# Performance work log

Hardware: AMD Instinct MI355X
Metric: run time of the kernel (lower is better)

## Reference

```python
import jax, jax.numpy as jnp
import numpy as np

B, S, D = 8, 2048, 768

def setup_inputs() -> dict:
    key = jax.random.key(0)
    k1, k2, k3, k4 = jax.random.split(key, 4)
    x = jax.random.normal(k1, (B, S, D), dtype=jnp.float32)
    # torch Linear stores weight as [out, in] and computes x @ W^T; we store
    # pre-transposed [in, out] matrices so forward is x @ W.
    scale = 1.0 / np.sqrt(D)
    wq = jax.random.normal(k2, (D, D), dtype=jnp.float32) * scale
    wk = jax.random.normal(k3, (D, D), dtype=jnp.float32) * scale
    wv = jax.random.normal(k4, (D, D), dtype=jnp.float32) * scale
    return {"x": x, "wq": wq, "wk": wk, "wv": wv}

def reference(x, wq, wk, wv):
    d_out = wq.shape[1]
    q = jnp.einsum('bsd,de->bse', x, wq)
    k = jnp.einsum('bsd,de->bse', x, wk)
    v = jnp.einsum('bsd,de->bse', x, wv)
    # causal scores: note source scales by sqrt(d_out), not per-head dim
    scores = jnp.einsum('bqe,bke->bqk', q, k) / jnp.sqrt(jnp.float32(d_out))
    S_len = x.shape[1]
    causal = jnp.tril(jnp.ones((S_len, S_len), dtype=bool))  # True = keep
    scores = jnp.where(causal[None, :, :], scores, -jnp.inf)
    attn = jax.nn.softmax(scores, axis=-1)
    # dropout rate = 0.0 -> identity
    out = jnp.einsum('bqk,bke->bqe', attn, v)
    return out
```

## Files before the change

### kernel.cpp

```cpp
#include <hip/hip_runtime.h>
#include <hip/hip_bf16.h>

#define DI 768
#define SS 2048
#define QK_ELEMS ((size_t)16384 * 768)

typedef float f32x4 __attribute__((ext_vector_type(4)));
typedef short s16x8 __attribute__((ext_vector_type(8)));
typedef short s16x4 __attribute__((ext_vector_type(4)));

static __device__ __forceinline__ unsigned short f2bf(float f) {
    union { float f; unsigned int u; } a; a.f = f;
    unsigned int r = (a.u + 0x7FFFu + ((a.u >> 16) & 1u)) >> 16;
    return (unsigned short)r;
}

#define GLOAD_LDS16(SRC, DST) \
    __builtin_amdgcn_global_load_lds((const __attribute__((address_space(1))) unsigned int*)(SRC), \
                                     (__attribute__((address_space(3))) unsigned int*)(DST), 16, 0, 0)

__global__ __launch_bounds__(256) void conv_kernel(
    const float* __restrict__ x, unsigned short* __restrict__ xb)
{
    const size_t i = ((size_t)blockIdx.x * 256 + threadIdx.x) * 8;
    float4 a = *(const float4*)(x + i);
    float4 c = *(const float4*)(x + i + 4);
    ushort4 u0, u1;
    u0.x = f2bf(a.x); u0.y = f2bf(a.y); u0.z = f2bf(a.z); u0.w = f2bf(a.w);
    u1.x = f2bf(c.x); u1.y = f2bf(c.y); u1.z = f2bf(c.z); u1.w = f2bf(c.w);
    *(ushort4*)(xb + i) = u0;
    *(ushort4*)(xb + i + 4) = u1;
}

__global__ __launch_bounds__(256) void convw_kernel(
    const float* __restrict__ wq, const float* __restrict__ wk,
    const float* __restrict__ wv, unsigned short* __restrict__ wtb)
{
    __shared__ float tile[64][65];
    const int which = blockIdx.z;
    const float* w = (which == 0) ? wq : (which == 1) ? wk : wv;
    unsigned short* o = wtb + (size_t)which * DI * DI;
    const int k0 = blockIdx.x * 64, n0 = blockIdx.y * 64;
    const int tid = threadIdx.x;
    #pragma unroll
    for (int i = 0; i < 16; ++i) {
        int idx = tid + i * 256;
        int rr = idx >> 6, cc = idx & 63;
        tile[rr][cc] = w[(size_t)(k0 + rr) * DI + n0 + cc];
    }
    __syncthreads();
    #pragma unroll
    for (int i = 0; i < 16; ++i) {
        int idx = tid + i * 256;
        int rr = idx >> 6, cc = idx & 63;
        o[(size_t)(n0 + rr) * DI + k0 + cc] = f2bf(tile[cc][rr]);
    }
}

__global__ __launch_bounds__(256) void proj_kernel(
    const unsigned short* __restrict__ xb, const unsigned short* __restrict__ wtb,
    unsigned short* __restrict__ ws)
{
    __shared__ unsigned short As[128 * 32];
    __shared__ unsigned short Bs[128 * 32];

    const int which = blockIdx.z;
    const unsigned short* wt = wtb + (size_t)which * DI * DI;
    const int n0 = blockIdx.x * 128;
    const int m0 = blockIdx.y * 128;
    const int tid = threadIdx.x;
    const int lane = tid & 63, wid = tid >> 6;
    const int wr = wid >> 1, wc = wid & 1;
    const int r = lane & 15, g = lane >> 4;

    const int arow_l = lane >> 2;
    const int asrc_l = (((lane & 3) * 16) ^ ((arow_l & 1) << 5)) >> 1;

    f32x4 acc[4][4];
    #pragma unroll
    for (int i = 0; i < 4; ++i)
        #pragma unroll
        for (int j = 0; j < 4; ++j) acc[i][j] = (f32x4){0.f, 0.f, 0.f, 0.f};

    for (int k0 = 0; k0 < DI; k0 += 32) {
        #pragma unroll
        for (int ii = 0; ii < 2; ++ii) {
            const int idx = wid * 2 + ii;
            GLOAD_LDS16(xb + (size_t)(m0 + idx * 16 + arow_l) * DI + k0 + asrc_l,
                        &As[idx * 512]);
            GLOAD_LDS16(wt + (size_t)(n0 + idx * 16 + arow_l) * DI + k0 + asrc_l,
                        &Bs[idx * 512]);
        }
        __syncthreads();
        s16x8 af[4], bfr[4];
        #pragma unroll
        for (int fr = 0; fr < 4; ++fr) {
            const int arow = wr * 64 + fr * 16 + r;
            af[fr] = *(const s16x8*)((const char*)As + arow * 64 + ((g * 16) ^ ((arow & 1) << 5)));
        }
        #pragma unroll
        for (int cf = 0; cf < 4; ++cf) {
            const int brow = wc * 64 + cf * 16 + r;
            bfr[cf] = *(const s16x8*)((const char*)Bs + brow * 64 + ((g * 16) ^ ((brow & 1) << 5)));
        }
        #pragma unroll
        for (int fr = 0; fr < 4; ++fr)
            #pragma unroll
            for (int cf = 0; cf < 4; ++cf)
                acc[fr][cf] = __builtin_amdgcn_mfma_f32_16x16x32_bf16(af[fr], bfr[cf], acc[fr][cf], 0, 0, 0);
        __syncthreads();
    }

    if (which == 0) {
        const float scale = 0.03608439182435161f;
        unsigned short* O = ws;
        #pragma unroll
        for (int fr = 0; fr < 4; ++fr)
            #pragma unroll
            for (int cf = 0; cf < 4; ++cf) {
                int row = m0 + wr * 64 + fr * 16 + g * 4;
                int col = n0 + wc * 64 + cf * 16 + r;
                #pragma unroll
                for (int jj = 0; jj < 4; ++jj) {
                    int q = row + jj;
                    O[((size_t)(q >> 5) * 96 + (col >> 3)) * 256 + (q & 31) * 8 + (col & 7)]
                        = f2bf(acc[fr][cf][jj] * scale);
                }
            }
    } else if (which == 1) {
        unsigned short* O = ws + QK_ELEMS;
        #pragma unroll
        for (int fr = 0; fr < 4; ++fr)
            #pragma unroll
            for (int cf = 0; cf < 4; ++cf) {
                int row = m0 + wr * 64 + fr * 16 + g * 4;
                int col = n0 + wc * 64 + cf * 16 + r;
                #pragma unroll
                for (int jj = 0; jj < 4; ++jj) {
                    int s = row + jj;
                    O[((size_t)(s >> 6) * 96 + (col >> 3)) * 512 + (s & 63) * 8 + (col & 7)]
                        = f2bf(acc[fr][cf][jj]);
                }
            }
    } else {
        unsigned short* O = ws + 2 * QK_ELEMS;
        #pragma unroll
        for (int fr = 0; fr < 4; ++fr)
            #pragma unroll
            for (int cf = 0; cf < 4; ++cf) {
                int row = m0 + wr * 64 + fr * 16 + g * 4;
                int bb = row >> 11;
                int st = (row & 2047) >> 4;
                int et = ((n0 + wc * 64) >> 4) + cf;
                ushort4 pk;
                pk.x = f2bf(acc[fr][cf][0]); pk.y = f2bf(acc[fr][cf][1]);
                pk.z = f2bf(acc[fr][cf][2]); pk.w = f2bf(acc[fr][cf][3]);
                *(ushort4*)&O[(((size_t)bb * 128 + st) * 48 + et) * 256 + lane * 4] = pk;
            }
    }
}

__global__ __launch_bounds__(512, 1) void attn_kernel(
    const unsigned short* __restrict__ ws, float* __restrict__ out)
{
    __shared__ unsigned short Ks[96 * 512];
    __shared__ unsigned short Qs[96 * 256];
    __shared__ unsigned short P_lds[2048];
    __shared__ float redm[128];

    const int id = blockIdx.x;
    const int b = id & 7;
    const int a = id >> 3;
    const int tid = threadIdx.x;
    const int wid = tid >> 6, lane = tid & 63;
    const int qsel = wid >> 2;
    const int wv = wid & 3;
    const int r = lane & 15, g = lane >> 4;
    const int et0 = wid * 6;
    const int rw = wv * 16 + r;

    const unsigned short* Qb = ws + (size_t)b * SS * DI;
    const unsigned short* Kb = ws + QK_ELEMS + (size_t)b * SS * DI;
    const unsigned short* Vf = ws + 2 * QK_ELEMS + (size_t)b * 128 * 48 * 256;
    float* Ob = out + (size_t)b * SS * DI;
    const char* KsB = (const char*)Ks;
    const char* QsB = (const char*)Qs;
    const int kfb = g * 1024 + rw * 16;
    const int qfb = g * 512 + (qsel * 16 + r) * 16;

#define STAGEK(KT) do { \
        const size_t sbase_ = (size_t)(KT) * 64 * DI; \
        _Pragma("unroll") \
        for (int i_ = 0; i_ < 12; ++i_) { \
            const int idx_ = wid * 12 + i_; \
            GLOAD_LDS16(Kb + sbase_ + idx_ * 512 + lane * 8, &Ks[idx_ * 512]); \
        } \
    } while (0)

#define RAWBAR() do { \
        asm volatile("s_waitcnt lgkmcnt(0)" ::: "memory"); \
        __builtin_amdgcn_sched_barrier(0); \
        __builtin_amdgcn_s_barrier(); \
        __builtin_amdgcn_sched_barrier(0); \
    } while (0)

    for (int pp = 0; pp < 2; ++pp) {
        const int jbase = pp ? (126 - 2 * a) : (2 * a);
        const int q0 = (jbase + qsel) * 16;
        const int nt0 = (jbase * 16 + 79) >> 6;
        const int ntmax = ((jbase + 1) * 16 + 79) >> 6;
        const int nt_own = qsel ? ntmax : nt0;

        {
            const size_t qsb = (size_t)jbase * 16 * DI;
            #pragma unroll
            for (int i_ = 0; i_ < 6; ++i_) {
                const int idx_ = wid * 6 + i_;
                GLOAD_LDS16(Qb + qsb + idx_ * 512 + lane * 8, &Qs[idx_ * 512]);
            }
        }
        STAGEK(0);

        f32x4 acc[2][6];
        #pragma unroll
        for (int qs = 0; qs < 2; ++qs)
            #pragma unroll
            for (int cf = 0; cf < 6; ++cf) acc[qs][cf] = (f32x4){0.f, 0.f, 0.f, 0.f};
        float m0 = -1e30f, m1 = -1e30f, lp = 0.f;

        for (int kt = 0; kt < ntmax; ++kt) {
            const int k0 = kt * 64;
            const bool act0 = kt < nt0;
            const bool act_own = kt < nt_own;
            __syncthreads();

            s16x4 va[4][6];
            const size_t vbase = ((size_t)(k0 >> 4) * 48 + et0) * 256 + lane * 4;
            #pragma unroll
            for (int ks = 0; ks < 4; ++ks)
                #pragma unroll
                for (int cf = 0; cf < 6; ++cf)
                    va[ks][cf] = *(const s16x4*)(Vf + vbase + (size_t)ks * 48 * 256 + cf * 256);

            f32x4 s = {0.f, 0.f, 0.f, 0.f};
            if (act_own) {
                f32x4 sa = {0,0,0,0}, sb = {0,0,0,0};
                __builtin_amdgcn_s_setprio(1);
                #pragma unroll
                for (int t = 0; t < 24; t += 2) {
                    s16x8 ka  = *(const s16x8*)(KsB + kfb + t * 4096);
                    s16x8 kb2 = *(const s16x8*)(KsB + kfb + t * 4096 + 4096);
                    s16x8 qa  = *(const s16x8*)(QsB + qfb + t * 2048);
                    s16x8 qb2 = *(const s16x8*)(QsB + qfb + t * 2048 + 2048);
                    sa = __builtin_amdgcn_mfma_f32_16x16x32_bf16(ka,  qa,  sa, 0, 0, 0);
                    sb = __builtin_amdgcn_mfma_f32_16x16x32_bf16(kb2, qb2, sb, 0, 0, 0);
                }
                __builtin_amdgcn_s_setprio(0);
                #pragma unroll
                for (int jj = 0; jj < 4; ++jj) s[jj] = sa[jj] + sb[jj];
                if (k0 + 64 > q0) {
                    #pragma unroll
                    for (int jj = 0; jj < 4; ++jj)
                        if (k0 + 16 * wv + 4 * g + jj > q0 + r) s[jj] = -1e30f;
                }
                float v = fmaxf(fmaxf(s[0], s[1]), fmaxf(s[2], s[3]));
                v = fmaxf(v, __shfl_xor(v, 16));
                v = fmaxf(v, __shfl_xor(v, 32));
                if (lane < 16) redm[qsel * 64 + wv * 16 + lane] = v;
            }
            RAWBAR();

            if (kt + 1 < ntmax) STAGEK(kt + 1);

            {
                float vm1 = fmaxf(fmaxf(redm[64 + r], redm[80 + r]),
                                  fmaxf(redm[96 + r], redm[112 + r]));
                float vm0 = act0 ? fmaxf(fmaxf(redm[r], redm[16 + r]),
                                         fmaxf(redm[32 + r], redm[48 + r])) : -1e30f;
                bool need = __any(vm1 > m1 + 8.0f) || (act0 && __any(vm0 > m0 + 8.0f));
                if (need) {
                    const float mn0 = fmaxf(m0, vm0), mn1 = fmaxf(m1, vm1);
                    const float a0 = __expf(m0 - mn0), a1 = __expf(m1 - mn1);
                    m0 = mn0; m1 = mn1;
                    lp *= qsel ? a1 : a0;
                    float al0[4], al1[4];
                    #pragma unroll
                    for (int jj = 0; jj < 4; ++jj) {
                        al0[jj] = __shfl(a0, 4 * g + jj);
                        al1[jj] = __shfl(a1, 4 * g + jj);
                    }
                    #pragma unroll
                    for (int cf = 0; cf < 6; ++cf)
                        #pragma unroll
                        for (int jj = 0; jj < 4; ++jj) {
                            acc[0][cf][jj] *= al0[jj];
                            acc[1][cf][jj] *= al1[jj];
                        }
                }
                if (act_own) {
                    const float mo = qsel ? m1 : m0;
                    s16x4 pw;
                    #pragma unroll
                    for (int jj = 0; jj < 4; ++jj) {
                        float p = __expf(s[jj] - mo);
                        lp += p;
                        pw[jj] = (short)f2bf(p);
                    }
                    *(s16x4*)&P_lds[qsel * 1024 + wv * 256 + r * 16 + g * 4] = pw;
                }
            }
            RAWBAR();

            {
                s16x4 pa0[4], pa1[4];
                #pragma unroll
                for (int ks = 0; ks < 4; ++ks) {
                    pa0[ks] = *(const s16x4*)&P_lds[ks * 256 + r * 16 + g * 4];
                    pa1[ks] = *(const s16x4*)&P_lds[1024 + ks * 256 + r * 16 + g * 4];
                }
                __builtin_amdgcn_s_setprio(1);
                if (act0) {
                    #pragma unroll
                    for (int cf = 0; cf < 6; ++cf)
                        #pragma unroll
                        for (int ks = 0; ks < 4; ++ks)
                            acc[0][cf] = __builtin_amdgcn_mfma_f32_16x16x16bf16_1k(pa0[ks], va[ks][cf], acc[0][cf], 0, 0, 0);
                }
                #pragma unroll
                for (int cf = 0; cf < 6; ++cf)
                    #pragma unroll
                    for (int ks = 0; ks < 4; ++ks)
                        acc[1][cf] = __builtin_amdgcn_mfma_f32_16x16x16bf16_1k(pa1[ks], va[ks][cf], acc[1][cf], 0, 0, 0);
                __builtin_amdgcn_s_setprio(0);
            }
        }
        lp += __shfl_xor(lp, 16);
        lp += __shfl_xor(lp, 32);
        if (lane < 16) redm[qsel * 64 + wv * 16 + lane] = lp;
        __syncthreads();
        const float lt0 = redm[r] + redm[16 + r] + redm[32 + r] + redm[48 + r];
        const float lt1 = redm[64 + r] + redm[80 + r] + redm[96 + r] + redm[112 + r];
        const float li0 = 1.0f / lt0, li1 = 1.0f / lt1;
        float lv0[4], lv1[4];
        #pragma unroll
        for (int jj = 0; jj < 4; ++jj) {
            lv0[jj] = __shfl(li0, 4 * g + jj);
            lv1[jj] = __shfl(li1, 4 * g + jj);
        }
        #pragma unroll
        for (int cf = 0; cf < 6; ++cf)
            #pragma unroll
            for (int jj = 0; jj < 4; ++jj) {
                Ob[(size_t)(jbase * 16 + 4 * g + jj) * DI + wid * 96 + cf * 16 + r] = acc[0][cf][jj] * lv0[jj];
                Ob[(size_t)((jbase + 1) * 16 + 4 * g + jj) * DI + wid * 96 + cf * 16 + r] = acc[1][cf][jj] * lv1[jj];
            }
        __syncthreads();
    }
#undef STAGEK
#undef RAWBAR
}

extern "C" void kernel_launch(void* const* d_in, const int* in_sizes, int n_in,
                              void* d_out, int out_size, void* d_ws, size_t ws_size,
                              hipStream_t stream) {
    const float* x  = (const float*)d_in[0];
    const float* wq = (const float*)d_in[1];
    const float* wk = (const float*)d_in[2];
    const float* wv = (const float*)d_in[3];
    unsigned short* ws = (unsigned short*)d_ws;
    float* out = (float*)d_out;
    unsigned short* xb  = (unsigned short*)d_out;
    unsigned short* wtb = (unsigned short*)d_out + QK_ELEMS;

    conv_kernel<<<(int)(QK_ELEMS / (256 * 8)), 256, 0, stream>>>(x, xb);
    convw_kernel<<<dim3(12, 12, 3), 256, 0, stream>>>(wq, wk, wv, wtb);
    proj_kernel<<<dim3(6, 128, 3), 256, 0, stream>>>(xb, wtb, ws);
    attn_kernel<<<256, 512, 0, stream>>>(ws, out);
}
```

Measured before the change: 259.5 us.

## Shrink attention tiles to 16 queries x 32 keys with 256-thread blocks, two per CU

Restructures the attention kernel so each block handles one 16-row query tile with 4 waves (256 threads) instead of two 16-row tiles with 8 waves, processing keys in 32-row chunks instead of 64. Q/K workspace layouts change to match the smaller tiles, and the grid doubles to 512 blocks with launch bounds allowing two blocks per CU. The aim is lower LDS use, better occupancy and load balance, and less wasted masked work on the causal diagonal. In exchange each key tile is reused across fewer query rows, V loads are issued per block with more iterations, only 2 of 4 waves compute scores, and there are more barriers per unit of work.

Result: slower. 312.8 us (+20.6%).

```diff
diff --git a/kernel.cpp b/kernel.cpp
--- a/kernel.cpp
+++ b/kernel.cpp
@@ -123,7 +123,7 @@
                 #pragma unroll
                 for (int jj = 0; jj < 4; ++jj) {
                     int q = row + jj;
-                    O[((size_t)(q >> 5) * 96 + (col >> 3)) * 256 + (q & 31) * 8 + (col & 7)]
+                    O[((size_t)(q >> 4) * 96 + (col >> 3)) * 128 + (q & 15) * 8 + (col & 7)]
                         = f2bf(acc[fr][cf][jj] * scale);
                 }
             }
@@ -138,7 +138,7 @@
                 #pragma unroll
                 for (int jj = 0; jj < 4; ++jj) {
                     int s = row + jj;
-                    O[((size_t)(s >> 6) * 96 + (col >> 3)) * 512 + (s & 63) * 8 + (col & 7)]
+                    O[((size_t)(s >> 5) * 96 + (col >> 3)) * 256 + (s & 31) * 8 + (col & 7)]
                         = f2bf(acc[fr][cf][jj]);
                 }
             }
@@ -160,24 +160,21 @@
     }
 }
 
-__global__ __launch_bounds__(512, 1) void attn_kernel(
+__global__ __launch_bounds__(256, 2) void attn_kernel(
     const unsigned short* __restrict__ ws, float* __restrict__ out)
 {
-    __shared__ unsigned short Ks[96 * 512];
-    __shared__ unsigned short Qs[96 * 256];
-    __shared__ unsigned short P_lds[2048];
-    __shared__ float redm[128];
+    __shared__ unsigned short Ks[96 * 256];
+    __shared__ unsigned short Qs[96 * 128];
+    __shared__ unsigned short P_lds[512];
+    __shared__ float redm[32];
 
     const int id = blockIdx.x;
     const int b = id & 7;
     const int a = id >> 3;
     const int tid = threadIdx.x;
     const int wid = tid >> 6, lane = tid & 63;
-    const int qsel = wid >> 2;
-    const int wv = wid & 3;
     const int r = lane & 15, g = lane >> 4;
-    const int et0 = wid * 6;
-    const int rw = wv * 16 + r;
+    const int et0 = wid * 12;
 
     const unsigned short* Qb = ws + (size_t)b * SS * DI;
     const unsigned short* Kb = ws + QK_ELEMS + (size_t)b * SS * DI;
@@ -185,11 +182,11 @@
     float* Ob = out + (size_t)b * SS * DI;
     const char* KsB = (const char*)Ks;
     const char* QsB = (const char*)Qs;
-    const int kfb = g * 1024 + rw * 16;
-    const int qfb = g * 512 + (qsel * 16 + r) * 16;
+    const int kfb = g * 512 + (wid * 16 + r) * 16;
+    const int qfb = g * 256 + r * 16;
 
 #define STAGEK(KT) do { \
-        const size_t sbase_ = (size_t)(KT) * 64 * DI; \
+        const size_t sbase_ = (size_t)(KT) * 32 * DI; \
         _Pragma("unroll") \
         for (int i_ = 0; i_ < 12; ++i_) { \
             const int idx_ = wid * 12 + i_; \
@@ -205,14 +202,12 @@
     } while (0)
 
     for (int pp = 0; pp < 2; ++pp) {
-        const int jbase = pp ? (126 - 2 * a) : (2 * a);
-        const int q0 = (jbase + qsel) * 16;
-        const int nt0 = (jbase * 16 + 79) >> 6;
-        const int ntmax = ((jbase + 1) * 16 + 79) >> 6;
-        const int nt_own = qsel ? ntmax : nt0;
+        const int j = pp ? (127 - a) : a;
+        const int q0 = j * 16;
+        const int nt = q0 / 32 + 1;
 
         {
-            const size_t qsb = (size_t)jbase * 16 * DI;
+            const size_t qsb = (size_t)j * 16 * DI;
             #pragma unroll
             for (int i_ = 0; i_ < 6; ++i_) {
                 const int idx_ = wid * 6 + i_;
@@ -221,139 +216,110 @@
         }
         STAGEK(0);
 
-        f32x4 acc[2][6];
-        #pragma unroll
-        for (int qs = 0; qs < 2; ++qs)
-            #pragma unroll
-            for (int cf = 0; cf < 6; ++cf) acc[qs][cf] = (f32x4){0.f, 0.f, 0.f, 0.f};
-        float m0 = -1e30f, m1 = -1e30f, lp = 0.f;
-
-        for (int kt = 0; kt < ntmax; ++kt) {
-            const int k0 = kt * 64;
-            const bool act0 = kt < nt0;
-            const bool act_own = kt < nt_own;
+        f32x4 acc[12];
+        #pragma unroll
+        for (int cf = 0; cf < 12; ++cf) acc[cf] = (f32x4){0.f, 0.f, 0.f, 0.f};
+        float m = -1e30f, lp = 0.f;
+
+        for (int kt = 0; kt < nt; ++kt) {
+            const int k0 = kt * 32;
             __syncthreads();
 
-            s16x4 va[4][6];
+            s16x4 va[2][12];
             const size_t vbase = ((size_t)(k0 >> 4) * 48 + et0) * 256 + lane * 4;
             #pragma unroll
-            for (int ks = 0; ks < 4; ++ks)
-                #pragma unroll
-                for (int cf = 0; cf < 6; ++cf)
+            for (int ks = 0; ks < 2; ++ks)
+                #pragma unroll
+                for (int cf = 0; cf < 12; ++cf)
                     va[ks][cf] = *(const s16x4*)(Vf + vbase + (size_t)ks * 48 * 256 + cf * 256);
 
             f32x4 s = {0.f, 0.f, 0.f, 0.f};
-            if (act_own) {
+            if (wid < 2) {
                 f32x4 sa = {0,0,0,0}, sb = {0,0,0,0};
                 __builtin_amdgcn_s_setprio(1);
                 #pragma unroll
                 for (int t = 0; t < 24; t += 2) {
-                    s16x8 ka  = *(const s16x8*)(KsB + kfb + t * 4096);
-                    s16x8 kb2 = *(const s16x8*)(KsB + kfb + t * 4096 + 4096);
-                    s16x8 qa  = *(const s16x8*)(QsB + qfb + t * 2048);
-                    s16x8 qb2 = *(const s16x8*)(QsB + qfb + t * 2048 + 2048);
+                    s16x8 ka  = *(const s16x8*)(KsB + kfb + t * 2048);
+                    s16x8 kb2 = *(const s16x8*)(KsB + kfb + t * 2048 + 2048);
+                    s16x8 qa  = *(const s16x8*)(QsB + qfb + t * 1024);
+                    s16x8 qb2 = *(const s16x8*)(QsB + qfb + t * 1024 + 1024);
                     sa = __builtin_amdgcn_mfma_f32_16x16x32_bf16(ka,  qa,  sa, 0, 0, 0);
                     sb = __builtin_amdgcn_mfma_f32_16x16x32_bf16(kb2, qb2, sb, 0, 0, 0);
                 }
                 __builtin_amdgcn_s_setprio(0);
                 #pragma unroll
                 for (int jj = 0; jj < 4; ++jj) s[jj] = sa[jj] + sb[jj];
-                if (k0 + 64 > q0) {
+                if (k0 + 32 > q0) {
                     #pragma unroll
                     for (int jj = 0; jj < 4; ++jj)
-                        if (k0 + 16 * wv + 4 * g + jj > q0 + r) s[jj] = -1e30f;
+                        if (k0 + 16 * wid + 4 * g + jj > q0 + r) s[jj] = -1e30f;
                 }
                 float v = fmaxf(fmaxf(s[0], s[1]), fmaxf(s[2], s[3]));
                 v = fmaxf(v, __shfl_xor(v, 16));
                 v = fmaxf(v, __shfl_xor(v, 32));
-                if (lane < 16) redm[qsel * 64 + wv * 16 + lane] = v;
+                if (lane < 16) redm[wid * 16 + lane] = v;
             }
             RAWBAR();
 
-            if (kt + 1 < ntmax) STAGEK(kt + 1);
+            if (kt + 1 < nt) STAGEK(kt + 1);
 
             {
-                float vm1 = fmaxf(fmaxf(redm[64 + r], redm[80 + r]),
-                                  fmaxf(redm[96 + r], redm[112 + r]));
-                float vm0 = act0 ? fmaxf(fmaxf(redm[r], redm[16 + r]),
-                                         fmaxf(redm[32 + r], redm[48 + r])) : -1e30f;
-                bool need = __any(vm1 > m1 + 8.0f) || (act0 && __any(vm0 > m0 + 8.0f));
-                if (need) {
-                    const float mn0 = fmaxf(m0, vm0), mn1 = fmaxf(m1, vm1);
-                    const float a0 = __expf(m0 - mn0), a1 = __expf(m1 - mn1);
-                    m0 = mn0; m1 = mn1;
-                    lp *= qsel ? a1 : a0;
-                    float al0[4], al1[4];
+                float vmax = fmaxf(redm[r], redm[16 + r]);
+                if (__any(vmax > m + 8.0f)) {
+                    const float mn = fmaxf(m, vmax);
+                    const float alpha = __expf(m - mn);
+                    m = mn;
+                    lp *= alpha;
+                    float al[4];
+                    #pragma unroll
+                    for (int jj = 0; jj < 4; ++jj) al[jj] = __shfl(alpha, 4 * g + jj);
+                    #pragma unroll
+                    for (int cf = 0; cf < 12; ++cf)
+                        #pragma unroll
+                        for (int jj = 0; jj < 4; ++jj) acc[cf][jj] *= al[jj];
+                }
+                if (wid < 2) {
+                    s16x4 pw;
                     #pragma unroll
                     for (int jj = 0; jj < 4; ++jj) {
-                        al0[jj] = __shfl(a0, 4 * g + jj);
-                        al1[jj] = __shfl(a1, 4 * g + jj);
-                    }
-                    #pragma unroll
-                    for (int cf = 0; cf < 6; ++cf)
-                        #pragma unroll
-                        for (int jj = 0; jj < 4; ++jj) {
-                            acc[0][cf][jj] *= al0[jj];
-                            acc[1][cf][jj] *= al1[jj];
-                        }
-                }
-                if (act_own) {
-                    const float mo = qsel ? m1 : m0;
-                    s16x4 pw;
-                    #pragma unroll
-                    for (int jj = 0; jj < 4; ++jj) {
-                        float p = __expf(s[jj] - mo);
+                        float p = __expf(s[jj] - m);
                         lp += p;
                         pw[jj] = (short)f2bf(p);
                     }
-                    *(s16x4*)&P_lds[qsel * 1024 + wv * 256 + r * 16 + g * 4] = pw;
+                    *(s16x4*)&P_lds[wid * 256 + r * 16 + g * 4] = pw;
                 }
             }
             RAWBAR();
 
             {
-                s16x4 pa0[4], pa1[4];
-                #pragma unroll
-                for (int ks = 0; ks < 4; ++ks) {
-                    pa0[ks] = *(const s16x4*)&P_lds[ks * 256 + r * 16 + g * 4];
-                    pa1[ks] = *(const s16x4*)&P_lds[1024 + ks * 256 + r * 16 + g * 4];
-                }
+                s16x4 pa[2];
+                pa[0] = *(const s16x4*)&P_lds[r * 16 + g * 4];
+                pa[1] = *(const s16x4*)&P_lds[256 + r * 16 + g * 4];
                 __builtin_amdgcn_s_setprio(1);
-                if (act0) {
-                    #pragma unroll
-                    for (int cf = 0; cf < 6; ++cf)
-                        #pragma unroll
-                        for (int ks = 0; ks < 4; ++ks)
-                            acc[0][cf] = __builtin_amdgcn_mfma_f32_16x16x16bf16_1k(pa0[ks], va[ks][cf], acc[0][cf], 0, 0, 0);
-                }
-                #pragma unroll
-                for (int cf = 0; cf < 6; ++cf)
-                    #pragma unroll
-                    for (int ks = 0; ks < 4; ++ks)
-                        acc[1][cf] = __builtin_amdgcn_mfma_f32_16x16x16bf16_1k(pa1[ks], va[ks][cf], acc[1][cf], 0, 0, 0);
+                #pragma unroll
+                for (int cf = 0; cf < 12; ++cf)
+                    #pragma unroll
+                    for (int ks = 0; ks < 2; ++ks)
+                        acc[cf] = __builtin_amdgcn_mfma_f32_16x16x16bf16_1k(pa[ks], va[ks][cf], acc[cf], 0, 0, 0);
                 __builtin_amdgcn_s_setprio(0);
             }
         }
-        lp += __shfl_xor(lp, 16);
-        lp += __shfl_xor(lp, 32);
-        if (lane < 16) redm[qsel * 64 + wv * 16 + lane] = lp;
+        if (wid < 2) {
+            lp += __shfl_xor(lp, 16);
+            lp += __shfl_xor(lp, 32);
+            if (lane < 16) redm[wid * 16 + lane] = lp;
+        }
         __syncthreads();
-        const float lt0 = redm[r] + redm[16 + r] + redm[32 + r] + redm[48 + r];
-        const float lt1 = redm[64 + r] + redm[80 + r] + redm[96 + r] + redm[112 + r];
-        const float li0 = 1.0f / lt0, li1 = 1.0f / lt1;
-        float lv0[4], lv1[4];
-        #pragma unroll
-        for (int jj = 0; jj < 4; ++jj) {
-            lv0[jj] = __shfl(li0, 4 * g + jj);
-            lv1[jj] = __shfl(li1, 4 * g + jj);
-        }
-        #pragma unroll
-        for (int cf = 0; cf < 6; ++cf)
-            #pragma unroll
-            for (int jj = 0; jj < 4; ++jj) {
-                Ob[(size_t)(jbase * 16 + 4 * g + jj) * DI + wid * 96 + cf * 16 + r] = acc[0][cf][jj] * lv0[jj];
-                Ob[(size_t)((jbase + 1) * 16 + 4 * g + jj) * DI + wid * 96 + cf * 16 + r] = acc[1][cf][jj] * lv1[jj];
-            }
+        const float lt = redm[r] + redm[16 + r];
+        const float linv = 1.0f / lt;
+        float lv[4];
+        #pragma unroll
+        for (int jj = 0; jj < 4; ++jj) lv[jj] = __shfl(linv, 4 * g + jj);
+        #pragma unroll
+        for (int cf = 0; cf < 12; ++cf)
+            #pragma unroll
+            for (int jj = 0; jj < 4; ++jj)
+                Ob[(size_t)(q0 + 4 * g + jj) * DI + wid * 192 + cf * 16 + r] = acc[cf][jj] * lv[jj];
         __syncthreads();
     }
 #undef STAGEK
@@ -375,5 +341,5 @@
     conv_kernel<<<(int)(QK_ELEMS / (256 * 8)), 256, 0, stream>>>(x, xb);
     convw_kernel<<<dim3(12, 12, 3), 256, 0, stream>>>(wq, wk, wv, wtb);
     proj_kernel<<<dim3(6, 128, 3), 256, 0, stream>>>(xb, wtb, ws);
-    attn_kernel<<<256, 512, 0, stream>>>(ws, out);
-}
+    attn_kernel<<<512, 256, 0, stream>>>(ws, out);
+}
```

## Prefetch next K tile through registers and merge conversion kernels

Applied to the files above, without the earlier changes.

The x and weight conversion kernels are merged into one prep kernel, saving a launch. In the attention loop, the next K tile is loaded from global memory into registers before the QK MFMA work and written to shared memory after the barrier. This replaces the direct global-to-LDS async load. The goal is to hide K load latency behind compute, at the cost of 12 extra vector registers per thread and extra barriers.

Measured after the change: 295.1 us. 1.14x slower.

```diff
diff --git a/kernel.cpp b/kernel.cpp
--- a/kernel.cpp
+++ b/kernel.cpp
@@ -19,41 +19,42 @@
     __builtin_amdgcn_global_load_lds((const __attribute__((address_space(1))) unsigned int*)(SRC), \
                                      (__attribute__((address_space(3))) unsigned int*)(DST), 16, 0, 0)
 
-__global__ __launch_bounds__(256) void conv_kernel(
-    const float* __restrict__ x, unsigned short* __restrict__ xb)
-{
-    const size_t i = ((size_t)blockIdx.x * 256 + threadIdx.x) * 8;
-    float4 a = *(const float4*)(x + i);
-    float4 c = *(const float4*)(x + i + 4);
-    ushort4 u0, u1;
-    u0.x = f2bf(a.x); u0.y = f2bf(a.y); u0.z = f2bf(a.z); u0.w = f2bf(a.w);
-    u1.x = f2bf(c.x); u1.y = f2bf(c.y); u1.z = f2bf(c.z); u1.w = f2bf(c.w);
-    *(ushort4*)(xb + i) = u0;
-    *(ushort4*)(xb + i + 4) = u1;
-}
-
-__global__ __launch_bounds__(256) void convw_kernel(
-    const float* __restrict__ wq, const float* __restrict__ wk,
-    const float* __restrict__ wv, unsigned short* __restrict__ wtb)
+__global__ __launch_bounds__(256) void prep_kernel(
+    const float* __restrict__ x, const float* __restrict__ wq,
+    const float* __restrict__ wk, const float* __restrict__ wv,
+    unsigned short* __restrict__ xb, unsigned short* __restrict__ wtb)
 {
     __shared__ float tile[64][65];
-    const int which = blockIdx.z;
-    const float* w = (which == 0) ? wq : (which == 1) ? wk : wv;
-    unsigned short* o = wtb + (size_t)which * DI * DI;
-    const int k0 = blockIdx.x * 64, n0 = blockIdx.y * 64;
+    const int bid = blockIdx.x;
     const int tid = threadIdx.x;
-    #pragma unroll
-    for (int i = 0; i < 16; ++i) {
-        int idx = tid + i * 256;
-        int rr = idx >> 6, cc = idx & 63;
-        tile[rr][cc] = w[(size_t)(k0 + rr) * DI + n0 + cc];
-    }
-    __syncthreads();
-    #pragma unroll
-    for (int i = 0; i < 16; ++i) {
-        int idx = tid + i * 256;
-        int rr = idx >> 6, cc = idx & 63;
-        o[(size_t)(n0 + rr) * DI + k0 + cc] = f2bf(tile[cc][rr]);
+    if (bid < 6144) {
+        const size_t i = ((size_t)bid * 256 + tid) * 8;
+        float4 a = *(const float4*)(x + i);
+        float4 c = *(const float4*)(x + i + 4);
+        ushort4 u0, u1;
+        u0.x = f2bf(a.x); u0.y = f2bf(a.y); u0.z = f2bf(a.z); u0.w = f2bf(a.w);
+        u1.x = f2bf(c.x); u1.y = f2bf(c.y); u1.z = f2bf(c.z); u1.w = f2bf(c.w);
+        *(ushort4*)(xb + i) = u0;
+        *(ushort4*)(xb + i + 4) = u1;
+    } else {
+        const int cid = bid - 6144;
+        const int which = cid / 144, rem = cid % 144;
+        const int k0 = (rem / 12) * 64, n0 = (rem % 12) * 64;
+        const float* w = (which == 0) ? wq : (which == 1) ? wk : wv;
+        unsigned short* o = wtb + (size_t)which * DI * DI;
+        #pragma unroll
+        for (int i = 0; i < 16; ++i) {
+            int idx = tid + i * 256;
+            int rr = idx >> 6, cc = idx & 63;
+            tile[rr][cc] = w[(size_t)(k0 + rr) * DI + n0 + cc];
+        }
+        __syncthreads();
+        #pragma unroll
+        for (int i = 0; i < 16; ++i) {
+            int idx = tid + i * 256;
+            int rr = idx >> 6, cc = idx & 63;
+            o[(size_t)(n0 + rr) * DI + k0 + cc] = f2bf(tile[cc][rr]);
+        }
     }
 }
 
@@ -188,15 +189,6 @@
     const int kfb = g * 1024 + rw * 16;
     const int qfb = g * 512 + (qsel * 16 + r) * 16;
 
-#define STAGEK(KT) do { \
-        const size_t sbase_ = (size_t)(KT) * 64 * DI; \
-        _Pragma("unroll") \
-        for (int i_ = 0; i_ < 12; ++i_) { \
-            const int idx_ = wid * 12 + i_; \
-            GLOAD_LDS16(Kb + sbase_ + idx_ * 512 + lane * 8, &Ks[idx_ * 512]); \
-        } \
-    } while (0)
-
 #define RAWBAR() do { \
         asm volatile("s_waitcnt lgkmcnt(0)" ::: "memory"); \
         __builtin_amdgcn_sched_barrier(0); \
@@ -218,8 +210,12 @@
                 const int idx_ = wid * 6 + i_;
                 GLOAD_LDS16(Qb + qsb + idx_ * 512 + lane * 8, &Qs[idx_ * 512]);
             }
-        }
-        STAGEK(0);
+            #pragma unroll
+            for (int i_ = 0; i_ < 12; ++i_) {
+                const int idx_ = wid * 12 + i_;
+                GLOAD_LDS16(Kb + idx_ * 512 + lane * 8, &Ks[idx_ * 512]);
+            }
+        }
 
         f32x4 acc[2][6];
         #pragma unroll
@@ -232,7 +228,10 @@
             const int k0 = kt * 64;
             const bool act0 = kt < nt0;
             const bool act_own = kt < nt_own;
-            __syncthreads();
+            const bool pf = (kt + 1 < ntmax);
+
+            if (kt == 0) __syncthreads();
+            else RAWBAR();
 
             s16x4 va[4][6];
             const size_t vbase = ((size_t)(k0 >> 4) * 48 + et0) * 256 + lane * 4;
@@ -242,9 +241,17 @@
                 for (int cf = 0; cf < 6; ++cf)
                     va[ks][cf] = *(const s16x4*)(Vf + vbase + (size_t)ks * 48 * 256 + cf * 256);
 
+            s16x8 kreg[12];
+            if (pf) {
+                const size_t sb = (size_t)(kt + 1) * 64 * DI;
+                #pragma unroll
+                for (int i_ = 0; i_ < 12; ++i_)
+                    kreg[i_] = *(const s16x8*)(Kb + sb + (wid * 12 + i_) * 512 + lane * 8);
+            }
+
             f32x4 s = {0.f, 0.f, 0.f, 0.f};
             if (act_own) {
-                f32x4 sa = {0,0,0,0}, sb = {0,0,0,0};
+                f32x4 sa = {0,0,0,0}, sb2 = {0,0,0,0};
                 __builtin_amdgcn_s_setprio(1);
                 #pragma unroll
                 for (int t = 0; t < 24; t += 2) {
@@ -252,12 +259,12 @@
                     s16x8 kb2 = *(const s16x8*)(KsB + kfb + t * 4096 + 4096);
                     s16x8 qa  = *(const s16x8*)(QsB + qfb + t * 2048);
                     s16x8 qb2 = *(const s16x8*)(QsB + qfb + t * 2048 + 2048);
-                    sa = __builtin_amdgcn_mfma_f32_16x16x32_bf16(ka,  qa,  sa, 0, 0, 0);
-                    sb = __builtin_amdgcn_mfma_f32_16x16x32_bf16(kb2, qb2, sb, 0, 0, 0);
+                    sa  = __builtin_amdgcn_mfma_f32_16x16x32_bf16(ka,  qa,  sa,  0, 0, 0);
+                    sb2 = __builtin_amdgcn_mfma_f32_16x16x32_bf16(kb2, qb2, sb2, 0, 0, 0);
                 }
                 __builtin_amdgcn_s_setprio(0);
                 #pragma unroll
-                for (int jj = 0; jj < 4; ++jj) s[jj] = sa[jj] + sb[jj];
+                for (int jj = 0; jj < 4; ++jj) s[jj] = sa[jj] + sb2[jj];
                 if (k0 + 64 > q0) {
                     #pragma unroll
                     for (int jj = 0; jj < 4; ++jj)
@@ -270,7 +277,11 @@
             }
             RAWBAR();
 
-            if (kt + 1 < ntmax) STAGEK(kt + 1);
+            if (pf) {
+                #pragma unroll
+                for (int i_ = 0; i_ < 12; ++i_)
+                    *(s16x8*)&Ks[(wid * 12 + i_) * 512 + lane * 8] = kreg[i_];
+            }
 
             {
                 float vm1 = fmaxf(fmaxf(redm[64 + r], redm[80 + r]),
@@ -356,7 +367,6 @@
             }
         __syncthreads();
     }
-#undef STAGEK
 #undef RAWBAR
 }
 
@@ -372,8 +382,7 @@
     unsigned short* xb  = (unsigned short*)d_out;
     unsigned short* wtb = (unsigned short*)d_out + QK_ELEMS;
 
-    conv_kernel<<<(int)(QK_ELEMS / (256 * 8)), 256, 0, stream>>>(x, xb);
-    convw_kernel<<<dim3(12, 12, 3), 256, 0, stream>>>(wq, wk, wv, wtb);
+    prep_kernel<<<6144 + 432, 256, 0, stream>>>(x, wq, wk, wv, xb, wtb);
     proj_kernel<<<dim3(6, 128, 3), 256, 0, stream>>>(xb, wtb, ws);
     attn_kernel<<<256, 512, 0, stream>>>(ws, out);
 }
```

## Double-buffer projection GEMM with larger 256x128 tiles and 8 warps

Applied to the files above, without the earlier changes.

Rewrites the QKV projection GEMM to use 512-thread blocks computing 256x128 output tiles with a 64-wide K step. LDS is double-buffered so the next K tile is fetched with global_load_lds while MFMAs run on the current one, and there is a single barrier per iteration plus an XOR swizzle and MFMA priority boosts. The goal is to hide global-load latency and raise arithmetic intensity in the projection stage. The cost is fewer blocks (1152 instead of 2304) with one block per CU, which may reduce occupancy-based latency hiding.

New measurement: 259.8 us. No clear change (+0.1%).

```diff
diff --git a/kernel.cpp b/kernel.cpp
--- a/kernel.cpp
+++ b/kernel.cpp
@@ -57,69 +57,95 @@
     }
 }
 
-__global__ __launch_bounds__(256) void proj_kernel(
+__global__ __launch_bounds__(512, 1) void proj_kernel(
     const unsigned short* __restrict__ xb, const unsigned short* __restrict__ wtb,
     unsigned short* __restrict__ ws)
 {
-    __shared__ unsigned short As[128 * 32];
-    __shared__ unsigned short Bs[128 * 32];
+    __shared__ unsigned short L[2 * 16384 + 2 * 8192];
 
     const int which = blockIdx.z;
     const unsigned short* wt = wtb + (size_t)which * DI * DI;
     const int n0 = blockIdx.x * 128;
-    const int m0 = blockIdx.y * 128;
+    const int m0 = blockIdx.y * 256;
     const int tid = threadIdx.x;
-    const int lane = tid & 63, wid = tid >> 6;
-    const int wr = wid >> 1, wc = wid & 1;
-    const int r = lane & 15, g = lane >> 4;
-
-    const int arow_l = lane >> 2;
-    const int asrc_l = (((lane & 3) * 16) ^ ((arow_l & 1) << 5)) >> 1;
-
-    f32x4 acc[4][4];
+    const int l = tid & 63, w = tid >> 6;
+    const int wm = w >> 2, wn = w & 3;
+    const int r = l & 15, g = l >> 4;
+
+    const int scol = ((l & 7) ^ ((l >> 3) & 7)) * 8;
+    const int srow = w * 16 + (l >> 3);
+
+    f32x4 acc[8][2];
     #pragma unroll
-    for (int i = 0; i < 4; ++i)
-        #pragma unroll
-        for (int j = 0; j < 4; ++j) acc[i][j] = (f32x4){0.f, 0.f, 0.f, 0.f};
-
-    for (int k0 = 0; k0 < DI; k0 += 32) {
-        #pragma unroll
-        for (int ii = 0; ii < 2; ++ii) {
-            const int idx = wid * 2 + ii;
-            GLOAD_LDS16(xb + (size_t)(m0 + idx * 16 + arow_l) * DI + k0 + asrc_l,
-                        &As[idx * 512]);
-            GLOAD_LDS16(wt + (size_t)(n0 + idx * 16 + arow_l) * DI + k0 + asrc_l,
-                        &Bs[idx * 512]);
+    for (int i = 0; i < 8; ++i) {
+        acc[i][0] = (f32x4){0.f, 0.f, 0.f, 0.f};
+        acc[i][1] = (f32x4){0.f, 0.f, 0.f, 0.f};
+    }
+
+#define STAGE_A(KT, H) do { \
+        const int b_ = (KT) & 1; \
+        _Pragma("unroll") \
+        for (int i_ = 0; i_ < 2; ++i_) \
+            GLOAD_LDS16(xb + (size_t)(m0 + (H) * 128 + srow + i_ * 8) * DI + (KT) * 64 + scol, \
+                        &L[b_ * 16384 + (H) * 8192 + w * 1024 + i_ * 512]); \
+    } while (0)
+#define STAGE_B(KT) do { \
+        const int b_ = (KT) & 1; \
+        _Pragma("unroll") \
+        for (int i_ = 0; i_ < 2; ++i_) \
+            GLOAD_LDS16(wt + (size_t)(n0 + srow + i_ * 8) * DI + (KT) * 64 + scol, \
+                        &L[32768 + b_ * 8192 + w * 1024 + i_ * 512]); \
+    } while (0)
+
+    STAGE_A(0, 0); STAGE_A(0, 1); STAGE_B(0);
+
+    for (int kt = 0; kt < 12; ++kt) {
+        const int b = kt & 1;
+        asm volatile("s_waitcnt vmcnt(0)" ::: "memory");
+        __builtin_amdgcn_sched_barrier(0);
+        __builtin_amdgcn_s_barrier();
+        __builtin_amdgcn_sched_barrier(0);
+
+        const unsigned short* Ab = &L[b * 16384];
+        const unsigned short* Bb = &L[32768 + b * 8192];
+        const bool pf = (kt + 1 < 12);
+
+        #pragma unroll
+        for (int q = 0; q < 4; ++q) {
+            if (pf) {
+                if (q == 0) STAGE_A(kt + 1, 0);
+                else if (q == 1) STAGE_A(kt + 1, 1);
+                else if (q == 2) STAGE_B(kt + 1);
+            }
+            const int kk = q >> 1, frh = q & 1;
+            const int koff = (kk * 32 + g * 8) ^ ((r & 7) << 3);
+            s16x8 af[4], bf[2];
+            #pragma unroll
+            for (int fr = 0; fr < 4; ++fr)
+                af[fr] = *(const s16x8*)&Ab[(wm * 128 + frh * 64 + fr * 16 + r) * 64 + koff];
+            #pragma unroll
+            for (int cf = 0; cf < 2; ++cf)
+                bf[cf] = *(const s16x8*)&Bb[(wn * 32 + cf * 16 + r) * 64 + koff];
+            __builtin_amdgcn_s_setprio(1);
+            #pragma unroll
+            for (int fr = 0; fr < 4; ++fr)
+                #pragma unroll
+                for (int cf = 0; cf < 2; ++cf)
+                    acc[frh * 4 + fr][cf] =
+                        __builtin_amdgcn_mfma_f32_16x16x32_bf16(af[fr], bf[cf], acc[frh * 4 + fr][cf], 0, 0, 0);
+            __builtin_amdgcn_s_setprio(0);
         }
-        __syncthreads();
-        s16x8 af[4], bfr[4];
-        #pragma unroll
-        for (int fr = 0; fr < 4; ++fr) {
-            const int arow = wr * 64 + fr * 16 + r;
-            af[fr] = *(const s16x8*)((const char*)As + arow * 64 + ((g * 16) ^ ((arow & 1) << 5)));
-        }
-        #pragma unroll
-        for (int cf = 0; cf < 4; ++cf) {
-            const int brow = wc * 64 + cf * 16 + r;
-            bfr[cf] = *(const s16x8*)((const char*)Bs + brow * 64 + ((g * 16) ^ ((brow & 1) << 5)));
-        }
-        #pragma unroll
-        for (int fr = 0; fr < 4; ++fr)
-            #pragma unroll
-            for (int cf = 0; cf < 4; ++cf)
-                acc[fr][cf] = __builtin_amdgcn_mfma_f32_16x16x32_bf16(af[fr], bfr[cf], acc[fr][cf], 0, 0, 0);
-        __syncthreads();
     }
 
     if (which == 0) {
         const float scale = 0.03608439182435161f;
         unsigned short* O = ws;
         #pragma unroll
-        for (int fr = 0; fr < 4; ++fr)
-            #pragma unroll
-            for (int cf = 0; cf < 4; ++cf) {
-                int row = m0 + wr * 64 + fr * 16 + g * 4;
-                int col = n0 + wc * 64 + cf * 16 + r;
+        for (int fr = 0; fr < 8; ++fr)
+            #pragma unroll
+            for (int cf = 0; cf < 2; ++cf) {
+                int row = m0 + wm * 128 + fr * 16 + g * 4;
+                int col = n0 + wn * 32 + cf * 16 + r;
                 #pragma unroll
                 for (int jj = 0; jj < 4; ++jj) {
                     int q = row + jj;
@@ -130,11 +156,11 @@
     } else if (which == 1) {
         unsigned short* O = ws + QK_ELEMS;
         #pragma unroll
-        for (int fr = 0; fr < 4; ++fr)
-            #pragma unroll
-            for (int cf = 0; cf < 4; ++cf) {
-                int row = m0 + wr * 64 + fr * 16 + g * 4;
-                int col = n0 + wc * 64 + cf * 16 + r;
+        for (int fr = 0; fr < 8; ++fr)
+            #pragma unroll
+            for (int cf = 0; cf < 2; ++cf) {
+                int row = m0 + wm * 128 + fr * 16 + g * 4;
+                int col = n0 + wn * 32 + cf * 16 + r;
                 #pragma unroll
                 for (int jj = 0; jj < 4; ++jj) {
                     int s = row + jj;
@@ -145,19 +171,21 @@
     } else {
         unsigned short* O = ws + 2 * QK_ELEMS;
         #pragma unroll
-        for (int fr = 0; fr < 4; ++fr)
-            #pragma unroll
-            for (int cf = 0; cf < 4; ++cf) {
-                int row = m0 + wr * 64 + fr * 16 + g * 4;
+        for (int fr = 0; fr < 8; ++fr)
+            #pragma unroll
+            for (int cf = 0; cf < 2; ++cf) {
+                int row = m0 + wm * 128 + fr * 16 + g * 4;
                 int bb = row >> 11;
                 int st = (row & 2047) >> 4;
-                int et = ((n0 + wc * 64) >> 4) + cf;
+                int et = ((n0 + wn * 32) >> 4) + cf;
                 ushort4 pk;
                 pk.x = f2bf(acc[fr][cf][0]); pk.y = f2bf(acc[fr][cf][1]);
                 pk.z = f2bf(acc[fr][cf][2]); pk.w = f2bf(acc[fr][cf][3]);
-                *(ushort4*)&O[(((size_t)bb * 128 + st) * 48 + et) * 256 + lane * 4] = pk;
-            }
-    }
+                *(ushort4*)&O[(((size_t)bb * 128 + st) * 48 + et) * 256 + l * 4] = pk;
+            }
+    }
+#undef STAGE_A
+#undef STAGE_B
 }
 
 __global__ __launch_bounds__(512, 1) void attn_kernel(
@@ -374,6 +402,6 @@
 
     conv_kernel<<<(int)(QK_ELEMS / (256 * 8)), 256, 0, stream>>>(x, xb);
     convw_kernel<<<dim3(12, 12, 3), 256, 0, stream>>>(wq, wk, wv, wtb);
-    proj_kernel<<<dim3(6, 128, 3), 256, 0, stream>>>(xb, wtb, ws);
+    proj_kernel<<<dim3(6, 64, 3), 512, 0, stream>>>(xb, wtb, ws);
     attn_kernel<<<256, 512, 0, stream>>>(ws, out);
 }
```
